# Performance work log

Measured on AMD Instinct MI355X. Metric: run time of the kernel, lower is better.

Reference implementation:

```python
import jax, jax.numpy as jnp
import numpy as np

N_NODES = 10000
N_EDGES = 320000
N_GRAPHS = 64
IN_DIM = 1
HID = 256


def setup_inputs() -> dict:
    key = jax.random.key(0)
    ks = jax.random.split(key, 12)
    s = 1.0 / np.sqrt(HID)
    inp = {
        "x": jax.random.normal(ks[0], (N_NODES, IN_DIM), dtype=jnp.float32),
        "edge_index": jax.random.randint(ks[1], (2, N_EDGES), 0, N_NODES, dtype=jnp.int64),
        "batch": jnp.sort(jax.random.randint(ks[2], (N_NODES,), 0, N_GRAPHS, dtype=jnp.int64)),
        "W_emb": jax.random.normal(ks[3], (IN_DIM, HID), dtype=jnp.float32),
        "b_emb": jnp.zeros((HID,), dtype=jnp.float32),
        "W1a": jax.random.normal(ks[4], (HID, HID), dtype=jnp.float32) * s,
        "b1a": jnp.zeros((HID,), dtype=jnp.float32),
        "W1b": jax.random.normal(ks[5], (HID, HID), dtype=jnp.float32) * s,
        "b1b": jnp.zeros((HID,), dtype=jnp.float32),
        "W2a": jax.random.normal(ks[6], (HID, HID), dtype=jnp.float32) * s,
        "b2a": jnp.zeros((HID,), dtype=jnp.float32),
        "W2b": jax.random.normal(ks[7], (HID, HID), dtype=jnp.float32) * s,
        "b2b": jnp.zeros((HID,), dtype=jnp.float32),
    }
    return inp


def _pointnet_conv(h, src, dst, Wa, ba, Wb, bb):
    # gather x_j -> 2-layer MLP per edge -> scatter-max at dst (PyG aggr='max')
    msg = jax.nn.relu(h[src] @ Wa + ba) @ Wb + bb          # [E, HID]
    agg = jax.ops.segment_max(msg, dst, num_segments=N_NODES)
    # PyG fills nodes with no incoming messages with 0
    return jnp.where(jnp.isneginf(agg), 0.0, agg)


def reference(x, edge_index, batch, W_emb, b_emb, W1a, b1a, W1b, b1b, W2a, b2a, W2b, b2b):
    src, dst = edge_index[0], edge_index[1]
    h = jax.nn.silu(x @ W_emb + b_emb)                     # [N, HID]
    h = h + jax.nn.silu(_pointnet_conv(h, src, dst, W1a, b1a, W1b, b1b))
    h = h + jax.nn.silu(_pointnet_conv(h, src, dst, W2a, b2a, W2b, b2b))
    # global_mean_pool over graphs
    sums = jax.ops.segment_sum(h, batch, num_segments=N_GRAPHS)          # [G, HID]
    cnts = jax.ops.segment_sum(jnp.ones((h.shape[0],), h.dtype), batch, num_segments=N_GRAPHS)
    return sums / jnp.maximum(cnts, 1.0)[:, None]
```

## Files before the change

### kernel.cpp

```cpp
#include <hip/hip_runtime.h>
#include <hip/hip_bf16.h>
#include <math.h>

#define HID 256
#define CAP 128
#define FB 64

typedef __attribute__((ext_vector_type(8))) short bf16x8;
typedef __attribute__((ext_vector_type(8))) unsigned short u16x8;
typedef __attribute__((ext_vector_type(4))) float f32x4;

__device__ __forceinline__ float silu_f(float z) {
    return z / (1.0f + __expf(-z));
}
__device__ __forceinline__ unsigned short f2bf(float f) {
    unsigned int u = __float_as_uint(f);
    u = (u + 0x7FFFu + ((u >> 16) & 1u)) >> 16;
    return (unsigned short)u;
}
__device__ __forceinline__ float bf2f(unsigned short b) {
    return __uint_as_float(((unsigned int)b) << 16);
}
__device__ __forceinline__ void max8(float m[8], u16x8 v) {
#pragma unroll
    for (int k = 0; k < 8; ++k) m[k] = fmaxf(m[k], bf2f(v[k]));
}

__global__ __launch_bounds__(256) void k_prep(
    const float* __restrict__ w0, const float* __restrict__ w1,
    const float* __restrict__ w2, const float* __restrict__ w3,
    unsigned short* __restrict__ o0, unsigned short* __restrict__ o1,
    unsigned short* __restrict__ o2, unsigned short* __restrict__ o3,
    const int* __restrict__ dst, int* __restrict__ cbase,
    const int* __restrict__ batch, int* __restrict__ goff,
    int N, int G, int E, int chunk) {
    __shared__ __align__(16) int shp[10000];
    int b = blockIdx.x;
    int tid = threadIdx.x;
    if (b < 64) {
        float (*ls)[65] = (float(*)[65])shp;
        int mat = b >> 4;
        int tile = b & 15;
        int k0 = (tile >> 2) * 64;
        int n0 = (tile & 3) * 64;
        const float* in = (mat == 0) ? w0 : (mat == 1) ? w1 : (mat == 2) ? w2 : w3;
        unsigned short* op = (mat == 0) ? o0 : (mat == 1) ? o1 : (mat == 2) ? o2 : o3;
        int lrb = tid >> 4;
        int lc = (tid & 15) * 4;
#pragma unroll
        for (int p = 0; p < 4; ++p) {
            int lr = p * 16 + lrb;
            float4 v = *(const float4*)(in + (size_t)(k0 + lr) * HID + n0 + lc);
            ls[lr][lc + 0] = v.x; ls[lr][lc + 1] = v.y;
            ls[lr][lc + 2] = v.z; ls[lr][lc + 3] = v.w;
        }
        __syncthreads();
#pragma unroll
        for (int p = 0; p < 4; ++p) {
            int ln = p * 16 + lrb;
            ushort4 q;
            q.x = f2bf(ls[lc + 0][ln]);
            q.y = f2bf(ls[lc + 1][ln]);
            q.z = f2bf(ls[lc + 2][ln]);
            q.w = f2bf(ls[lc + 3][ln]);
            *(ushort4*)(op + (size_t)(n0 + ln) * HID + k0 + lc) = q;
        }
    } else if (b == 64) {
        int g = tid;
        if (g > G) return;
        int lo = 0, hi = N;
        while (lo < hi) {
            int mid = (lo + hi) >> 1;
            if (batch[mid] < g) lo = mid + 1; else hi = mid;
        }
        goff[g] = lo;
    } else {
        int fb = b - 65;
        int* hist = shp;
        for (int i = tid; i < N; i += 256) hist[i] = 0;
        __syncthreads();
        int e0 = fb * chunk;
        int e1 = min(E, e0 + chunk);
        for (int e = e0 + tid * 4; e + 3 < e1; e += 1024) {
            int4 d4 = *(const int4*)(dst + e);
            atomicAdd(&hist[d4.x], 1);
            atomicAdd(&hist[d4.y], 1);
            atomicAdd(&hist[d4.z], 1);
            atomicAdd(&hist[d4.w], 1);
        }
        int rem = (e1 - e0) & 3;
        if (tid < rem) atomicAdd(&hist[dst[e1 - rem + tid]], 1);
        __syncthreads();
        for (int i = tid; i < N; i += 256) cbase[(size_t)fb * N + i] = hist[i];
    }
}

__global__ __launch_bounds__(256) void k_prefix(int* __restrict__ cbase,
                                                int* __restrict__ cnt, int N) {
    int d = blockIdx.x * 256 + threadIdx.x;
    if (d >= N) return;
    int run = 0;
#pragma unroll
    for (int b = 0; b < FB; ++b) {
        int c = cbase[(size_t)b * N + d];
        cbase[(size_t)b * N + d] = run;
        run += c;
    }
    cnt[d] = run;
}

__global__ __launch_bounds__(256) void k_mlp1f(
    const float* __restrict__ x, const float* __restrict__ Wemb,
    const float* __restrict__ bemb,
    const unsigned short* __restrict__ Wta, const float* __restrict__ ba,
    const unsigned short* __restrict__ Wtb, const float* __restrict__ bbv,
    unsigned short* __restrict__ hb, unsigned short* __restrict__ t2,
    const int* __restrict__ src, const int* __restrict__ dst,
    const int* __restrict__ cbase, unsigned short* __restrict__ csr,
    int M, int E, int MT, int chunk) {
    __shared__ __align__(16) int shbuf[10000];
    unsigned short (*As)[264]  = (unsigned short(*)[264])shbuf;
    unsigned short (*t1s)[264] = (unsigned short(*)[264])((char*)shbuf + 16896);
    int b = blockIdx.x;
    int tid = threadIdx.x;

    if (b >= MT) {
        int fb = b - MT;
        int* hist = shbuf;
        for (int i = tid; i < M; i += 256) hist[i] = 0;
        __syncthreads();
        int e0 = fb * chunk;
        int e1 = min(E, e0 + chunk);
        const int* cb = cbase + (size_t)fb * M;
        for (int e = e0 + tid * 4; e + 3 < e1; e += 1024) {
            int4 d4 = *(const int4*)(dst + e);
            int4 s4 = *(const int4*)(src + e);
            int r0 = atomicAdd(&hist[d4.x], 1);
            int r1 = atomicAdd(&hist[d4.y], 1);
            int r2 = atomicAdd(&hist[d4.z], 1);
            int r3 = atomicAdd(&hist[d4.w], 1);
            int p0 = cb[d4.x] + r0;
            int p1 = cb[d4.y] + r1;
            int p2 = cb[d4.z] + r2;
            int p3 = cb[d4.w] + r3;
            if (p0 < CAP) csr[d4.x * CAP + p0] = (unsigned short)s4.x;
            if (p1 < CAP) csr[d4.y * CAP + p1] = (unsigned short)s4.y;
            if (p2 < CAP) csr[d4.z * CAP + p2] = (unsigned short)s4.z;
            if (p3 < CAP) csr[d4.w * CAP + p3] = (unsigned short)s4.w;
        }
        int rem = (e1 - e0) & 3;
        if (tid < rem) {
            int e = e1 - rem + tid;
            int d = dst[e];
            int r = atomicAdd(&hist[d], 1);
            int p = cb[d] + r;
            if (p < CAP) csr[d * CAP + p] = (unsigned short)src[e];
        }
        return;
    }

    int lane = tid & 63;
    int wave = tid >> 6;
    int quad = lane >> 4;
    int r = lane & 15;
    int m0 = b * 32;
    int colw = wave * 64;

    {
        int row = tid >> 3;
        int c0 = (tid & 7) * 32;
        int grow = m0 + row;
        float xv = (grow < M) ? x[grow] : 0.0f;
#pragma unroll
        for (int j = 0; j < 8; ++j) {
            int c = c0 + j * 4;
            ushort4 q;
            q.x = f2bf(silu_f(xv * Wemb[c + 0] + bemb[c + 0]));
            q.y = f2bf(silu_f(xv * Wemb[c + 1] + bemb[c + 1]));
            q.z = f2bf(silu_f(xv * Wemb[c + 2] + bemb[c + 2]));
            q.w = f2bf(silu_f(xv * Wemb[c + 3] + bemb[c + 3]));
            if (grow < M) *(ushort4*)(hb + (size_t)grow * HID + c) = q;
            *(ushort4*)&As[row][c] = q;
        }
        __syncthreads();
    }

    f32x4 acc[2][4];
#pragma unroll
    for (int rt = 0; rt < 2; ++rt)
#pragma unroll
        for (int nt = 0; nt < 4; ++nt) acc[rt][nt] = (f32x4)0.0f;
#pragma unroll
    for (int ks = 0; ks < 8; ++ks) {
        bf16x8 a0 = *(const bf16x8*)&As[r][ks * 32 + quad * 8];
        bf16x8 a1 = *(const bf16x8*)&As[r + 16][ks * 32 + quad * 8];
#pragma unroll
        for (int nt = 0; nt < 4; ++nt) {
            bf16x8 bfr = *(const bf16x8*)(Wta + (size_t)(colw + nt * 16 + r) * HID
                                          + ks * 32 + quad * 8);
            acc[0][nt] = __builtin_amdgcn_mfma_f32_16x16x32_bf16(a0, bfr, acc[0][nt], 0, 0, 0);
            acc[1][nt] = __builtin_amdgcn_mfma_f32_16x16x32_bf16(a1, bfr, acc[1][nt], 0, 0, 0);
        }
    }
#pragma unroll
    for (int nt = 0; nt < 4; ++nt) {
        int col = colw + nt * 16 + r;
        float bv = ba[col];
#pragma unroll
        for (int rt = 0; rt < 2; ++rt)
#pragma unroll
            for (int i = 0; i < 4; ++i) {
                float v = fmaxf(acc[rt][nt][i] + bv, 0.0f);
                t1s[rt * 16 + quad * 4 + i][col] = f2bf(v);
            }
    }
    __syncthreads();

    f32x4 acc2[2][4];
#pragma unroll
    for (int rt = 0; rt < 2; ++rt)
#pragma unroll
        for (int nt = 0; nt < 4; ++nt) acc2[rt][nt] = (f32x4)0.0f;
#pragma unroll
    for (int ks = 0; ks < 8; ++ks) {
        bf16x8 a0 = *(const bf16x8*)&t1s[r][ks * 32 + quad * 8];
        bf16x8 a1 = *(const bf16x8*)&t1s[r + 16][ks * 32 + quad * 8];
#pragma unroll
        for (int nt = 0; nt < 4; ++nt) {
            bf16x8 bfr = *(const bf16x8*)(Wtb + (size_t)(colw + nt * 16 + r) * HID
                                          + ks * 32 + quad * 8);
            acc2[0][nt] = __builtin_amdgcn_mfma_f32_16x16x32_bf16(a0, bfr, acc2[0][nt], 0, 0, 0);
            acc2[1][nt] = __builtin_amdgcn_mfma_f32_16x16x32_bf16(a1, bfr, acc2[1][nt], 0, 0, 0);
        }
    }
#pragma unroll
    for (int nt = 0; nt < 4; ++nt) {
        int col = colw + nt * 16 + r;
        float bv = bbv[col];
#pragma unroll
        for (int rt = 0; rt < 2; ++rt)
#pragma unroll
            for (int i = 0; i < 4; ++i) {
                int row = m0 + rt * 16 + quad * 4 + i;
                if (row < M) t2[(size_t)row * HID + col] = f2bf(acc2[rt][nt][i] + bv);
            }
    }
}

__global__ __launch_bounds__(256) void k_mlp2(
    const unsigned short* __restrict__ Aglob,
    const unsigned short* __restrict__ Wta, const float* __restrict__ ba,
    const unsigned short* __restrict__ Wtb, const float* __restrict__ bbv,
    unsigned short* __restrict__ t2, int M) {
    __shared__ unsigned short t1s[32][264];
    int tid = threadIdx.x;
    int lane = tid & 63;
    int wave = tid >> 6;
    int quad = lane >> 4;
    int r = lane & 15;
    int m0 = blockIdx.x * 32;
    int colw = wave * 64;

    f32x4 acc[2][4];
#pragma unroll
    for (int rt = 0; rt < 2; ++rt)
#pragma unroll
        for (int nt = 0; nt < 4; ++nt) acc[rt][nt] = (f32x4)0.0f;

    int ar0 = m0 + r;        if (ar0 >= M) ar0 = M - 1;
    int ar1 = m0 + 16 + r;   if (ar1 >= M) ar1 = M - 1;

#pragma unroll
    for (int ks = 0; ks < 8; ++ks) {
        bf16x8 a0 = *(const bf16x8*)(Aglob + (size_t)ar0 * HID + ks * 32 + quad * 8);
        bf16x8 a1 = *(const bf16x8*)(Aglob + (size_t)ar1 * HID + ks * 32 + quad * 8);
#pragma unroll
        for (int nt = 0; nt < 4; ++nt) {
            bf16x8 bfr = *(const bf16x8*)(Wta + (size_t)(colw + nt * 16 + r) * HID
                                          + ks * 32 + quad * 8);
            acc[0][nt] = __builtin_amdgcn_mfma_f32_16x16x32_bf16(a0, bfr, acc[0][nt], 0, 0, 0);
            acc[1][nt] = __builtin_amdgcn_mfma_f32_16x16x32_bf16(a1, bfr, acc[1][nt], 0, 0, 0);
        }
    }
#pragma unroll
    for (int nt = 0; nt < 4; ++nt) {
        int col = colw + nt * 16 + r;
        float bv = ba[col];
#pragma unroll
        for (int rt = 0; rt < 2; ++rt)
#pragma unroll
            for (int i = 0; i < 4; ++i) {
                float v = fmaxf(acc[rt][nt][i] + bv, 0.0f);
                t1s[rt * 16 + quad * 4 + i][col] = f2bf(v);
            }
    }
    __syncthreads();

    f32x4 acc2[2][4];
#pragma unroll
    for (int rt = 0; rt < 2; ++rt)
#pragma unroll
        for (int nt = 0; nt < 4; ++nt) acc2[rt][nt] = (f32x4)0.0f;
#pragma unroll
    for (int ks = 0; ks < 8; ++ks) {
        bf16x8 a0 = *(const bf16x8*)&t1s[r][ks * 32 + quad * 8];
        bf16x8 a1 = *(const bf16x8*)&t1s[r + 16][ks * 32 + quad * 8];
#pragma unroll
        for (int nt = 0; nt < 4; ++nt) {
            bf16x8 bfr = *(const bf16x8*)(Wtb + (size_t)(colw + nt * 16 + r) * HID
                                          + ks * 32 + quad * 8);
            acc2[0][nt] = __builtin_amdgcn_mfma_f32_16x16x32_bf16(a0, bfr, acc2[0][nt], 0, 0, 0);
            acc2[1][nt] = __builtin_amdgcn_mfma_f32_16x16x32_bf16(a1, bfr, acc2[1][nt], 0, 0, 0);
        }
    }
#pragma unroll
    for (int nt = 0; nt < 4; ++nt) {
        int col = colw + nt * 16 + r;
        float bv = bbv[col];
#pragma unroll
        for (int rt = 0; rt < 2; ++rt)
#pragma unroll
            for (int i = 0; i < 4; ++i) {
                int row = m0 + rt * 16 + quad * 4 + i;
                if (row < M) t2[(size_t)row * HID + col] = f2bf(acc2[rt][nt][i] + bv);
            }
    }
}

__global__ __launch_bounds__(256) void k_agg(const unsigned short* __restrict__ t2,
                                             const int* __restrict__ cnt,
                                             const unsigned short* __restrict__ csr,
                                             unsigned short* __restrict__ hb, int N) {
    int lane = threadIdx.x & 63;
    int node = (blockIdx.x * blockDim.x + threadIdx.x) >> 6;
    if (node >= N) return;
    int half = lane >> 5;
    int lc = (lane & 31) * 8;
    const unsigned short* base = t2 + lc;

    int deg = cnt[node];
    if (deg > CAP) deg = CAP;
    const unsigned short* rowp = csr + (size_t)node * CAP;
    size_t o = (size_t)node * HID + lc;
    u16x8 hq = *(const u16x8*)(hb + o);

    float m[8];
#pragma unroll
    for (int k = 0; k < 8; ++k) m[k] = -INFINITY;

    int i = 0;
    for (; i + 16 <= deg; i += 16) {
        int s[8];
#pragma unroll
        for (int j = 0; j < 8; ++j) s[j] = rowp[i + 2 * j + half];
        u16x8 v[8];
#pragma unroll
        for (int j = 0; j < 8; ++j) v[j] = *(const u16x8*)(base + (size_t)s[j] * HID);
#pragma unroll
        for (int j = 0; j < 8; ++j) max8(m, v[j]);
    }
    if (i + 8 <= deg) {
        int s[4];
#pragma unroll
        for (int j = 0; j < 4; ++j) s[j] = rowp[i + 2 * j + half];
        u16x8 v[4];
#pragma unroll
        for (int j = 0; j < 4; ++j) v[j] = *(const u16x8*)(base + (size_t)s[j] * HID);
#pragma unroll
        for (int j = 0; j < 4; ++j) max8(m, v[j]);
        i += 8;
    }
    for (; i < deg; i += 2) {
        int idx = i + half; if (idx >= deg) idx = deg - 1;
        int s = rowp[idx];
        u16x8 v = *(const u16x8*)(base + (size_t)s * HID);
        max8(m, v);
    }

#pragma unroll
    for (int k = 0; k < 8; ++k) m[k] = fmaxf(m[k], __shfl_xor(m[k], 32, 64));
    if (deg == 0) {
#pragma unroll
        for (int k = 0; k < 8; ++k) m[k] = 0.0f;
    }

    if (half == 0) {
        u16x8 q;
#pragma unroll
        for (int k = 0; k < 8; ++k) q[k] = f2bf(bf2f(hq[k]) + silu_f(m[k]));
        *(u16x8*)(hb + o) = q;
    }
}

__global__ __launch_bounds__(1024) void k_pool(const unsigned short* __restrict__ hb,
                                               const int* __restrict__ goff,
                                               float* __restrict__ out) {
    __shared__ float part[3][HID];
    int g = blockIdx.x;
    int tid = threadIdx.x;
    int c = tid & 255;
    int chunk = tid >> 8;
    int beg = goff[g], end = goff[g + 1];
    float s = 0.f;
    for (int n = beg + chunk; n < end; n += 4) s += bf2f(hb[(size_t)n * HID + c]);
    if (chunk > 0) part[chunk - 1][c] = s;
    __syncthreads();
    if (chunk == 0) {
        s += part[0][c] + part[1][c] + part[2][c];
        int cnt = end - beg;
        out[g * HID + c] = s / (float)(cnt > 0 ? cnt : 1);
    }
}

extern "C" void kernel_launch(void* const* d_in, const int* in_sizes, int n_in,
                              void* d_out, int out_size, void* d_ws, size_t ws_size,
                              hipStream_t stream) {
    const float* x     = (const float*)d_in[0];
    const int*   ei    = (const int*)d_in[1];
    const int*   batch = (const int*)d_in[2];
    const float* Wemb  = (const float*)d_in[3];
    const float* bemb  = (const float*)d_in[4];
    const float* W1a   = (const float*)d_in[5];
    const float* b1a   = (const float*)d_in[6];
    const float* W1b   = (const float*)d_in[7];
    const float* b1b   = (const float*)d_in[8];
    const float* W2a   = (const float*)d_in[9];
    const float* b2a   = (const float*)d_in[10];
    const float* W2b   = (const float*)d_in[11];
    const float* b2b   = (const float*)d_in[12];
    float* out = (float*)d_out;

    const int N = in_sizes[0];
    const int E = in_sizes[1] / 2;
    const int G = out_size / HID;
    const int* src = ei;
    const int* dst = ei + E;

    char* ws = (char*)d_ws;
    unsigned short* hb   = (unsigned short*)ws; ws += (size_t)N * HID * 2;
    unsigned short* t2   = (unsigned short*)ws; ws += (size_t)N * HID * 2;
    unsigned short* Wt1a = (unsigned short*)ws; ws += (size_t)HID * HID * 2;
    unsigned short* Wt1b = (unsigned short*)ws; ws += (size_t)HID * HID * 2;
    unsigned short* Wt2a = (unsigned short*)ws; ws += (size_t)HID * HID * 2;
    unsigned short* Wt2b = (unsigned short*)ws; ws += (size_t)HID * HID * 2;
    int* cnt   = (int*)ws; ws += (size_t)N * 4;
    int* goff  = (int*)ws; ws += (size_t)(G + 1) * 4;
    int* cbase = (int*)ws; ws += (size_t)FB * N * 4;
    unsigned short* csr = (unsigned short*)ws; ws += (size_t)N * CAP * 2;

    const int chunk = (((E + FB - 1) / FB) + 3) & ~3;
    const int MT = (N + 31) / 32;

    k_prep<<<64 + 1 + FB, 256, 0, stream>>>(W1a, W1b, W2a, W2b,
                                            Wt1a, Wt1b, Wt2a, Wt2b,
                                            dst, cbase, batch, goff, N, G, E, chunk);

    k_prefix<<<(N + 255) / 256, 256, 0, stream>>>(cbase, cnt, N);

    k_mlp1f<<<MT + FB, 256, 0, stream>>>(x, Wemb, bemb, Wt1a, b1a, Wt1b, b1b,
                                         hb, t2, src, dst, cbase, csr, N, E, MT, chunk);

    int agg_blocks = (N * 64 + 255) / 256;

    k_agg<<<agg_blocks, 256, 0, stream>>>(t2, cnt, csr, hb, N);

    k_mlp2<<<MT, 256, 0, stream>>>(hb, Wt2a, b2a, Wt2b, b2b, t2, N);

    k_agg<<<agg_blocks, 256, 0, stream>>>(t2, cnt, csr, hb, N);

    k_pool<<<G, 1024, 0, stream>>>(hb, goff, out);
}
```

Measured before the change: 194.7 us.

## Fuse first aggregation into layer-2 MLP kernel and pack 16-bit LDS histograms

The first max-aggregation is fused into the layer-2 MLP kernel. Each block aggregates its 32 nodes into shared memory and feeds them straight to the MFMA GEMM, which removes a kernel launch and the global round trip of the aggregated features. A new t3 buffer avoids overwriting t2 while other blocks still read it. The edge histograms now pack two 16-bit counters per 32-bit LDS word, halving shared memory and the zeroing work, and the aggregation loop is unrolled to 32 gathers. The risk is lower parallelism in the fused kernel (one block of 4 waves now aggregates 32 nodes serially, 8 per wave) and higher register pressure.

```diff
diff --git a/kernel.cpp b/kernel.cpp
--- a/kernel.cpp
+++ b/kernel.cpp
@@ -24,6 +24,76 @@
 __device__ __forceinline__ void max8(float m[8], u16x8 v) {
 #pragma unroll
     for (int k = 0; k < 8; ++k) m[k] = fmaxf(m[k], bf2f(v[k]));
+}
+
+__device__ __forceinline__ void agg_one(const unsigned short* __restrict__ msg,
+                                        const int* __restrict__ cnt,
+                                        const unsigned short* __restrict__ csr,
+                                        unsigned short* __restrict__ hb,
+                                        unsigned short* as_row,
+                                        int node, int lane) {
+    int half = lane >> 5;
+    int lc = (lane & 31) * 8;
+    const unsigned short* base = msg + lc;
+
+    int deg = cnt[node];
+    if (deg > CAP) deg = CAP;
+    const unsigned short* rowp = csr + (size_t)node * CAP;
+    size_t o = (size_t)node * HID + lc;
+    u16x8 hq = *(const u16x8*)(hb + o);
+
+    float m[8];
+#pragma unroll
+    for (int k = 0; k < 8; ++k) m[k] = -INFINITY;
+
+    int i = 0;
+    for (; i + 32 <= deg; i += 32) {
+        int s[16];
+#pragma unroll
+        for (int j = 0; j < 16; ++j) s[j] = rowp[i + 2 * j + half];
+        u16x8 v[16];
+#pragma unroll
+        for (int j = 0; j < 16; ++j) v[j] = *(const u16x8*)(base + (size_t)s[j] * HID);
+#pragma unroll
+        for (int j = 0; j < 16; ++j) max8(m, v[j]);
+    }
+    for (; i + 16 <= deg; i += 16) {
+        int s[8];
+#pragma unroll
+        for (int j = 0; j < 8; ++j) s[j] = rowp[i + 2 * j + half];
+        u16x8 v[8];
+#pragma unroll
+        for (int j = 0; j < 8; ++j) v[j] = *(const u16x8*)(base + (size_t)s[j] * HID);
+#pragma unroll
+        for (int j = 0; j < 8; ++j) max8(m, v[j]);
+    }
+    if (i < deg) {
+        int s[8];
+#pragma unroll
+        for (int j = 0; j < 8; ++j) {
+            int idx = i + 2 * j + half; if (idx >= deg) idx = deg - 1;
+            s[j] = rowp[idx];
+        }
+        u16x8 v[8];
+#pragma unroll
+        for (int j = 0; j < 8; ++j) v[j] = *(const u16x8*)(base + (size_t)s[j] * HID);
+#pragma unroll
+        for (int j = 0; j < 8; ++j) max8(m, v[j]);
+    }
+
+#pragma unroll
+    for (int k = 0; k < 8; ++k) m[k] = fmaxf(m[k], __shfl_xor(m[k], 32, 64));
+    if (deg == 0) {
+#pragma unroll
+        for (int k = 0; k < 8; ++k) m[k] = 0.0f;
+    }
+    if (half == 0) {
+        u16x8 q;
+#pragma unroll
+        for (int k = 0; k < 8; ++k) q[k] = f2bf(bf2f(hq[k]) + silu_f(m[k]));
+        *(u16x8*)(hb + o) = q;
+        if (as_row) *(u16x8*)(as_row + lc) = q;
+    }
 }
 
 __global__ __launch_bounds__(256) void k_prep(
@@ -34,7 +104,7 @@
     const int* __restrict__ dst, int* __restrict__ cbase,
     const int* __restrict__ batch, int* __restrict__ goff,
     int N, int G, int E, int chunk) {
-    __shared__ __align__(16) int shp[10000];
+    __shared__ __align__(16) unsigned int shp[5000];
     int b = blockIdx.x;
     int tid = threadIdx.x;
     if (b < 64) {
@@ -76,22 +146,27 @@
         goff[g] = lo;
     } else {
         int fb = b - 65;
-        int* hist = shp;
-        for (int i = tid; i < N; i += 256) hist[i] = 0;
+        unsigned int* hist = shp;
+        int N2 = (N + 1) >> 1;
+        for (int i = tid; i < N2; i += 256) hist[i] = 0u;
         __syncthreads();
         int e0 = fb * chunk;
         int e1 = min(E, e0 + chunk);
         for (int e = e0 + tid * 4; e + 3 < e1; e += 1024) {
             int4 d4 = *(const int4*)(dst + e);
-            atomicAdd(&hist[d4.x], 1);
-            atomicAdd(&hist[d4.y], 1);
-            atomicAdd(&hist[d4.z], 1);
-            atomicAdd(&hist[d4.w], 1);
+            atomicAdd(&hist[d4.x >> 1], 1u << ((d4.x & 1) * 16));
+            atomicAdd(&hist[d4.y >> 1], 1u << ((d4.y & 1) * 16));
+            atomicAdd(&hist[d4.z >> 1], 1u << ((d4.z & 1) * 16));
+            atomicAdd(&hist[d4.w >> 1], 1u << ((d4.w & 1) * 16));
         }
         int rem = (e1 - e0) & 3;
-        if (tid < rem) atomicAdd(&hist[dst[e1 - rem + tid]], 1);
+        if (tid < rem) {
+            int d = dst[e1 - rem + tid];
+            atomicAdd(&hist[d >> 1], 1u << ((d & 1) * 16));
+        }
         __syncthreads();
-        for (int i = tid; i < N; i += 256) cbase[(size_t)fb * N + i] = hist[i];
+        for (int i = tid; i < N; i += 256)
+            cbase[(size_t)fb * N + i] = (int)((hist[i >> 1] >> ((i & 1) * 16)) & 0xffffu);
     }
 }
 
@@ -100,7 +175,6 @@
     int d = blockIdx.x * 256 + threadIdx.x;
     if (d >= N) return;
     int run = 0;
-#pragma unroll
     for (int b = 0; b < FB; ++b) {
         int c = cbase[(size_t)b * N + d];
         cbase[(size_t)b * N + d] = run;
@@ -118,7 +192,7 @@
     const int* __restrict__ src, const int* __restrict__ dst,
     const int* __restrict__ cbase, unsigned short* __restrict__ csr,
     int M, int E, int MT, int chunk) {
-    __shared__ __align__(16) int shbuf[10000];
+    __shared__ __align__(16) unsigned int shbuf[8448];
     unsigned short (*As)[264]  = (unsigned short(*)[264])shbuf;
     unsigned short (*t1s)[264] = (unsigned short(*)[264])((char*)shbuf + 16896);
     int b = blockIdx.x;
@@ -126,8 +200,9 @@
 
     if (b >= MT) {
         int fb = b - MT;
-        int* hist = shbuf;
-        for (int i = tid; i < M; i += 256) hist[i] = 0;
+        unsigned int* hist = shbuf;
+        int N2 = (M + 1) >> 1;
+        for (int i = tid; i < N2; i += 256) hist[i] = 0u;
         __syncthreads();
         int e0 = fb * chunk;
         int e1 = min(E, e0 + chunk);
@@ -135,14 +210,14 @@
         for (int e = e0 + tid * 4; e + 3 < e1; e += 1024) {
             int4 d4 = *(const int4*)(dst + e);
             int4 s4 = *(const int4*)(src + e);
-            int r0 = atomicAdd(&hist[d4.x], 1);
-            int r1 = atomicAdd(&hist[d4.y], 1);
-            int r2 = atomicAdd(&hist[d4.z], 1);
-            int r3 = atomicAdd(&hist[d4.w], 1);
-            int p0 = cb[d4.x] + r0;
-            int p1 = cb[d4.y] + r1;
-            int p2 = cb[d4.z] + r2;
-            int p3 = cb[d4.w] + r3;
+            unsigned int o0 = atomicAdd(&hist[d4.x >> 1], 1u << ((d4.x & 1) * 16));
+            unsigned int o1 = atomicAdd(&hist[d4.y >> 1], 1u << ((d4.y & 1) * 16));
+            unsigned int o2 = atomicAdd(&hist[d4.z >> 1], 1u << ((d4.z & 1) * 16));
+            unsigned int o3 = atomicAdd(&hist[d4.w >> 1], 1u << ((d4.w & 1) * 16));
+            int p0 = cb[d4.x] + (int)((o0 >> ((d4.x & 1) * 16)) & 0xffffu);
+            int p1 = cb[d4.y] + (int)((o1 >> ((d4.y & 1) * 16)) & 0xffffu);
+            int p2 = cb[d4.z] + (int)((o2 >> ((d4.z & 1) * 16)) & 0xffffu);
+            int p3 = cb[d4.w] + (int)((o3 >> ((d4.w & 1) * 16)) & 0xffffu);
             if (p0 < CAP) csr[d4.x * CAP + p0] = (unsigned short)s4.x;
             if (p1 < CAP) csr[d4.y * CAP + p1] = (unsigned short)s4.y;
             if (p2 < CAP) csr[d4.z * CAP + p2] = (unsigned short)s4.z;
@@ -152,8 +227,8 @@
         if (tid < rem) {
             int e = e1 - rem + tid;
             int d = dst[e];
-            int r = atomicAdd(&hist[d], 1);
-            int p = cb[d] + r;
+            unsigned int ov = atomicAdd(&hist[d >> 1], 1u << ((d & 1) * 16));
+            int p = cb[d] + (int)((ov >> ((d & 1) * 16)) & 0xffffu);
             if (p < CAP) csr[d * CAP + p] = (unsigned short)src[e];
         }
         return;
@@ -247,11 +322,13 @@
     }
 }
 
-__global__ __launch_bounds__(256) void k_mlp2(
-    const unsigned short* __restrict__ Aglob,
+__global__ __launch_bounds__(256) void k_mlp2agg(
+    const unsigned short* __restrict__ msg, const int* __restrict__ cnt,
+    const unsigned short* __restrict__ csr, unsigned short* __restrict__ hb,
     const unsigned short* __restrict__ Wta, const float* __restrict__ ba,
     const unsigned short* __restrict__ Wtb, const float* __restrict__ bbv,
-    unsigned short* __restrict__ t2, int M) {
+    unsigned short* __restrict__ t3, int M) {
+    __shared__ unsigned short As[32][264];
     __shared__ unsigned short t1s[32][264];
     int tid = threadIdx.x;
     int lane = tid & 63;
@@ -261,19 +338,22 @@
     int m0 = blockIdx.x * 32;
     int colw = wave * 64;
 
+    for (int t = 0; t < 8; ++t) {
+        int row = wave * 8 + t;
+        int node = m0 + row;
+        if (node < M) agg_one(msg, cnt, csr, hb, &As[row][0], node, lane);
+    }
+    __syncthreads();
+
     f32x4 acc[2][4];
 #pragma unroll
     for (int rt = 0; rt < 2; ++rt)
 #pragma unroll
         for (int nt = 0; nt < 4; ++nt) acc[rt][nt] = (f32x4)0.0f;
-
-    int ar0 = m0 + r;        if (ar0 >= M) ar0 = M - 1;
-    int ar1 = m0 + 16 + r;   if (ar1 >= M) ar1 = M - 1;
-
 #pragma unroll
     for (int ks = 0; ks < 8; ++ks) {
-        bf16x8 a0 = *(const bf16x8*)(Aglob + (size_t)ar0 * HID + ks * 32 + quad * 8);
-        bf16x8 a1 = *(const bf16x8*)(Aglob + (size_t)ar1 * HID + ks * 32 + quad * 8);
+        bf16x8 a0 = *(const bf16x8*)&As[r][ks * 32 + quad * 8];
+        bf16x8 a1 = *(const bf16x8*)&As[r + 16][ks * 32 + quad * 8];
 #pragma unroll
         for (int nt = 0; nt < 4; ++nt) {
             bf16x8 bfr = *(const bf16x8*)(Wta + (size_t)(colw + nt * 16 + r) * HID
@@ -322,74 +402,19 @@
 #pragma unroll
             for (int i = 0; i < 4; ++i) {
                 int row = m0 + rt * 16 + quad * 4 + i;
-                if (row < M) t2[(size_t)row * HID + col] = f2bf(acc2[rt][nt][i] + bv);
+                if (row < M) t3[(size_t)row * HID + col] = f2bf(acc2[rt][nt][i] + bv);
             }
     }
 }
 
-__global__ __launch_bounds__(256) void k_agg(const unsigned short* __restrict__ t2,
+__global__ __launch_bounds__(256) void k_agg(const unsigned short* __restrict__ msg,
                                              const int* __restrict__ cnt,
                                              const unsigned short* __restrict__ csr,
                                              unsigned short* __restrict__ hb, int N) {
     int lane = threadIdx.x & 63;
     int node = (blockIdx.x * blockDim.x + threadIdx.x) >> 6;
     if (node >= N) return;
-    int half = lane >> 5;
-    int lc = (lane & 31) * 8;
-    const unsigned short* base = t2 + lc;
-
-    int deg = cnt[node];
-    if (deg > CAP) deg = CAP;
-    const unsigned short* rowp = csr + (size_t)node * CAP;
-    size_t o = (size_t)node * HID + lc;
-    u16x8 hq = *(const u16x8*)(hb + o);
-
-    float m[8];
-#pragma unroll
-    for (int k = 0; k < 8; ++k) m[k] = -INFINITY;
-
-    int i = 0;
-    for (; i + 16 <= deg; i += 16) {
-        int s[8];
-#pragma unroll
-        for (int j = 0; j < 8; ++j) s[j] = rowp[i + 2 * j + half];
-        u16x8 v[8];
-#pragma unroll
-        for (int j = 0; j < 8; ++j) v[j] = *(const u16x8*)(base + (size_t)s[j] * HID);
-#pragma unroll
-        for (int j = 0; j < 8; ++j) max8(m, v[j]);
-    }
-    if (i + 8 <= deg) {
-        int s[4];
-#pragma unroll
-        for (int j = 0; j < 4; ++j) s[j] = rowp[i + 2 * j + half];
-        u16x8 v[4];
-#pragma unroll
-        for (int j = 0; j < 4; ++j) v[j] = *(const u16x8*)(base + (size_t)s[j] * HID);
-#pragma unroll
-        for (int j = 0; j < 4; ++j) max8(m, v[j]);
-        i += 8;
-    }
-    for (; i < deg; i += 2) {
-        int idx = i + half; if (idx >= deg) idx = deg - 1;
-        int s = rowp[idx];
-        u16x8 v = *(const u16x8*)(base + (size_t)s * HID);
-        max8(m, v);
-    }
-
-#pragma unroll
-    for (int k = 0; k < 8; ++k) m[k] = fmaxf(m[k], __shfl_xor(m[k], 32, 64));
-    if (deg == 0) {
-#pragma unroll
-        for (int k = 0; k < 8; ++k) m[k] = 0.0f;
-    }
-
-    if (half == 0) {
-        u16x8 q;
-#pragma unroll
-        for (int k = 0; k < 8; ++k) q[k] = f2bf(bf2f(hq[k]) + silu_f(m[k]));
-        *(u16x8*)(hb + o) = q;
-    }
+    agg_one(msg, cnt, csr, hb, (unsigned short*)0, node, lane);
 }
 
 __global__ __launch_bounds__(1024) void k_pool(const unsigned short* __restrict__ hb,
@@ -439,6 +464,7 @@
     char* ws = (char*)d_ws;
     unsigned short* hb   = (unsigned short*)ws; ws += (size_t)N * HID * 2;
     unsigned short* t2   = (unsigned short*)ws; ws += (size_t)N * HID * 2;
+    unsigned short* t3   = (unsigned short*)ws; ws += (size_t)N * HID * 2;
     unsigned short* Wt1a = (unsigned short*)ws; ws += (size_t)HID * HID * 2;
     unsigned short* Wt1b = (unsigned short*)ws; ws += (size_t)HID * HID * 2;
     unsigned short* Wt2a = (unsigned short*)ws; ws += (size_t)HID * HID * 2;
@@ -460,13 +486,11 @@
     k_mlp1f<<<MT + FB, 256, 0, stream>>>(x, Wemb, bemb, Wt1a, b1a, Wt1b, b1b,
                                          hb, t2, src, dst, cbase, csr, N, E, MT, chunk);
 
+    k_mlp2agg<<<MT, 256, 0, stream>>>(t2, cnt, csr, hb,
+                                      Wt2a, b2a, Wt2b, b2b, t3, N);
+
     int agg_blocks = (N * 64 + 255) / 256;
-
-    k_agg<<<agg_blocks, 256, 0, stream>>>(t2, cnt, csr, hb, N);
-
-    k_mlp2<<<MT, 256, 0, stream>>>(hb, Wt2a, b2a, Wt2b, b2b, t2, N);
-
-    k_agg<<<agg_blocks, 256, 0, stream>>>(t2, cnt, csr, hb, N);
+    k_agg<<<agg_blocks, 256, 0, stream>>>(t3, cnt, csr, hb, N);
 
     k_pool<<<G, 1024, 0, stream>>>(hb, goff, out);
 }
```

After: 192.5 us. About the same (-1.1%).
